# Kernel tuning notes

Measured on AMD Instinct MI355X. Metric: run time of the kernel, lower is better.

## Reference

```python
import jax, jax.numpy as jnp
import numpy as np

N = 50000


def gcn_conv(x, edge_index, W, b):
    # x: [N, F_in], edge_index: [2, E] (row=source j, col=target i)
    n = x.shape[0]
    loops = jnp.arange(n, dtype=edge_index.dtype)
    row = jnp.concatenate([edge_index[0], loops])
    col = jnp.concatenate([edge_index[1], loops])
    # linear transform first (PyG GCNConv)
    xw = x @ W  # [N, F_out]
    # symmetric normalization deg^{-1/2}[row] * deg^{-1/2}[col]
    deg = jax.ops.segment_sum(jnp.ones_like(col, dtype=xw.dtype), col, num_segments=n)
    dis = jnp.where(deg > 0, jax.lax.rsqrt(jnp.maximum(deg, 1e-12)), 0.0)
    norm = dis[row] * dis[col]  # [E+N]
    # gather-scale-scatter: sum_j norm_ij * (W x_j)
    msgs = xw[row] * norm[:, None]
    out = jax.ops.segment_sum(msgs, col, num_segments=n)
    return out + b


def setup_inputs() -> dict:
    key = jax.random.key(0)
    k1, k2, k3, k4, k5 = jax.random.split(key, 5)
    in_dim, hidden_dim, out_dim = 128, 128, 64
    x = jax.random.normal(k1, (N, in_dim), dtype=jnp.float32)
    edge_index = jax.random.randint(k2, (2, 800000), 0, N, dtype=jnp.int64)
    s1 = 1.0 / np.sqrt(in_dim)
    s2 = 1.0 / np.sqrt(hidden_dim)
    W1 = jax.random.uniform(k3, (in_dim, hidden_dim), jnp.float32, -s1, s1)
    b1 = jnp.zeros((hidden_dim,), jnp.float32)
    W2 = jax.random.uniform(k4, (hidden_dim, out_dim), jnp.float32, -s2, s2)
    b2 = jnp.zeros((out_dim,), jnp.float32)
    return {"x": x, "edge_index": edge_index, "W1": W1, "b1": b1, "W2": W2, "b2": b2}


def reference(x, edge_index, W1, b1, W2, b2):
    h = gcn_conv(x, edge_index, W1, b1)
    h = jax.nn.relu(h)
    # dropout(p=0.5, training=False) -> identity (inference reference)
    out = gcn_conv(h, edge_index, W2, b2)
    return out
```

## Files before the change

### kernel.cpp

```cpp
#include <hip/hip_runtime.h>
#include <hip/hip_fp16.h>


typedef _Float16 half8 __attribute__((ext_vector_type(8)));
typedef float floatx4 __attribute__((ext_vector_type(4)));

__global__ void k_count(const int* __restrict__ col, int* __restrict__ deg,
                        int* __restrict__ rank, int E) {
    int e = blockIdx.x * blockDim.x + threadIdx.x;
    if (e < E) rank[e] = atomicAdd(&deg[col[e]], 1);
}

__global__ __launch_bounds__(1024) void k_scan_local(const int* __restrict__ deg,
                                                     int* __restrict__ rowptr,
                                                     int* __restrict__ bsum,
                                                     float* __restrict__ dis, int n) {
    __shared__ int wsum[16];
    int b = blockIdx.x, tid = threadIdx.x;
    int lane = tid & 63, w = tid >> 6;
    int i = b * 1024 + tid;
    int v = (i < n) ? deg[i] : 0;
    if (i < n) dis[i] = rsqrtf((float)v + 1.0f);
    int sc = v;
#pragma unroll
    for (int off = 1; off < 64; off <<= 1) {
        int t = __shfl_up(sc, off);
        if (lane >= off) sc += t;
    }
    if (lane == 63) wsum[w] = sc;
    __syncthreads();
    if (w == 0) {
        int s = (lane < 16) ? wsum[lane] : 0;
#pragma unroll
        for (int off = 1; off < 16; off <<= 1) {
            int t = __shfl_up(s, off);
            if (lane >= off) s += t;
        }
        if (lane < 16) wsum[lane] = s;
    }
    __syncthreads();
    int incl = sc + ((w > 0) ? wsum[w - 1] : 0);
    if (i < n) rowptr[i + 1] = incl;
    if (tid == 1023) bsum[b] = incl;
    if (b == 0 && tid == 0) rowptr[0] = 0;
}

template <int N, typename AT>
__device__ __forceinline__ void gemm_tile(const AT* __restrict__ X,
                                          const float* __restrict__ W,
                                          const float* __restrict__ scale,
                                          __half* __restrict__ Y, int M,
                                          int m0, __half2* wt, int tid) {
    for (int i = tid; i < N * 64; i += 256) {
        int nn = i & (N - 1);
        int k2 = i / N;
        float w0 = W[(size_t)(2 * k2) * N + nn];
        float w1 = W[(size_t)(2 * k2 + 1) * N + nn];
        wt[nn * 64 + ((k2 >> 2) ^ (nn & 15)) * 4 + (k2 & 3)] = __floats2half2_rn(w0, w1);
    }
    __syncthreads();
    int wid = tid >> 6, lane = tid & 63;
    int col = lane & 15, quad = lane >> 4;
    int m_a = m0 + wid * 16 + col;
    bool a_ok = m_a < M;
    constexpr int NT = N / 16;
    floatx4 acc[NT] = {};
#pragma unroll
    for (int ks = 0; ks < 4; ++ks) {
        int k = ks * 32 + quad * 8;
        half8 af;
        if constexpr (sizeof(AT) == 4) {
            floatx4 a0 = {0.f, 0.f, 0.f, 0.f}, a1 = {0.f, 0.f, 0.f, 0.f};
            if (a_ok) {
                a0 = *(const floatx4*)&X[(size_t)m_a * 128 + k];
                a1 = *(const floatx4*)&X[(size_t)m_a * 128 + k + 4];
            }
            af = half8{(_Float16)a0[0], (_Float16)a0[1], (_Float16)a0[2], (_Float16)a0[3],
                       (_Float16)a1[0], (_Float16)a1[1], (_Float16)a1[2], (_Float16)a1[3]};
        } else {
            half8 t = {};
            if (a_ok) t = *(const half8*)(const void*)&X[(size_t)m_a * 128 + k];
            af = t;
        }
        int kblk = ks * 4 + quad;
#pragma unroll
        for (int nt = 0; nt < NT; ++nt) {
            int nn = nt * 16 + col;
            half8 bf = *(const half8*)(const void*)&wt[nn * 64 + (kblk ^ (nn & 15)) * 4];
            acc[nt] = __builtin_amdgcn_mfma_f32_16x16x32_f16(af, bf, acc[nt], 0, 0, 0);
        }
    }
    int mbase = m0 + wid * 16 + quad * 4;
    float s[4];
#pragma unroll
    for (int r = 0; r < 4; ++r) s[r] = (mbase + r < M) ? scale[mbase + r] : 0.f;
#pragma unroll
    for (int nt = 0; nt < NT; ++nt) {
#pragma unroll
        for (int r = 0; r < 4; ++r) {
            if (mbase + r < M)
                Y[(size_t)(mbase + r) * N + nt * 16 + col] = __float2half(acc[nt][r] * s[r]);
        }
    }
}

__global__ __launch_bounds__(256) void k_fix_gemm1(int* __restrict__ rowptr,
                                                   const int* __restrict__ bsum, int n,
                                                   const float* __restrict__ X,
                                                   const float* __restrict__ W,
                                                   const float* __restrict__ scale,
                                                   __half* __restrict__ Y, int M, int FB) {
    __shared__ __align__(16) __half2 wt[128 * 64];
    int b = blockIdx.x, tid = threadIdx.x;
    if (b < FB) {
        int* red = (int*)wt;
        int partial = 0;
        for (int j = tid; j < b; j += 256) partial += bsum[j];
        red[tid] = partial;
        __syncthreads();
        for (int off = 128; off > 0; off >>= 1) {
            if (tid < off) red[tid] += red[tid + off];
            __syncthreads();
        }
        int offv = red[0];
        if (offv == 0) return;
#pragma unroll
        for (int r = 0; r < 4; ++r) {
            int i = b * 1024 + r * 256 + tid;
            if (i < n) rowptr[i + 1] += offv;
        }
        return;
    }
    gemm_tile<128, float>(X, W, scale, Y, M, (b - FB) * 64, wt, tid);
}

__global__ __launch_bounds__(256) void k_gemm2(const __half* __restrict__ X,
                                               const float* __restrict__ W,
                                               const float* __restrict__ scale,
                                               __half* __restrict__ Y, int M) {
    __shared__ __align__(16) __half2 wt[64 * 64];
    gemm_tile<64, __half>(X, W, scale, Y, M, blockIdx.x * 64, wt, threadIdx.x);
}

__global__ void k_fill(const int* __restrict__ row, const int* __restrict__ col,
                       const int* __restrict__ rowptr, const int* __restrict__ rank,
                       int* __restrict__ csr, int E) {
    int e = blockIdx.x * blockDim.x + threadIdx.x;
    if (e < E) csr[rowptr[col[e]] + rank[e]] = row[e];
}

__global__ __launch_bounds__(256) void k_agg128(const __half* __restrict__ xw,
                                                const float* __restrict__ dis,
                                                const int* __restrict__ rowptr,
                                                const int* __restrict__ csr,
                                                const float* __restrict__ bias,
                                                __half* __restrict__ out, int n) {
    int tid = threadIdx.x;
    int lane = tid & 63;
    int q = lane >> 4, li = lane & 15;
    int qbase = lane & 48;
    int node = blockIdx.x * 16 + ((tid >> 6) << 2) + q;
    bool ok = node < n;
    float di = 0.f;
    int beg = 0, end = 0;
    if (ok) {
        di = dis[node];
        beg = rowptr[node];
        end = rowptr[node + 1];
    }
    int dg = end - beg;
    int m1 = max(dg, __shfl(dg, lane ^ 16));
    int mx = max(m1, __shfl(m1, lane ^ 32));
    const half8* rows = (const half8*)xw;
    float acc[8] = {};
    if (ok) {
        half8 sf = rows[(size_t)node * 16 + li];
#pragma unroll
        for (int f = 0; f < 8; ++f) acc[f] = (float)sf[f];
    }
    for (int i = 0; i < mx; i += 8) {
        int e = beg + i + (li & 7);
        int myidx = (e < end) ? csr[e] : 0;
        half8 v[8];
#pragma unroll
        for (int j = 0; j < 8; ++j) {
            int s = __shfl(myidx, qbase + j);
            v[j] = rows[(size_t)s * 16 + li];
        }
#pragma unroll
        for (int j = 0; j < 8; ++j) {
            if (beg + i + j < end) {
#pragma unroll
                for (int f = 0; f < 8; ++f) acc[f] += (float)v[j][f];
            }
        }
    }
    if (ok) {
        floatx4 b0 = *(const floatx4*)&bias[li * 8];
        floatx4 b1 = *(const floatx4*)&bias[li * 8 + 4];
        half8 o;
#pragma unroll
        for (int f = 0; f < 4; ++f) o[f] = (_Float16)fmaxf(acc[f] * di + b0[f], 0.f);
#pragma unroll
        for (int f = 0; f < 4; ++f) o[4 + f] = (_Float16)fmaxf(acc[4 + f] * di + b1[f], 0.f);
        ((half8*)out)[(size_t)node * 16 + li] = o;
    }
}

__global__ __launch_bounds__(256) void k_agg64(const __half* __restrict__ xw,
                                               const float* __restrict__ dis,
                                               const int* __restrict__ rowptr,
                                               const int* __restrict__ csr,
                                               const float* __restrict__ bias,
                                               float* __restrict__ out, int n) {
    int tid = threadIdx.x;
    int lane = tid & 63;
    int o8 = lane >> 3, li = lane & 7;
    int obase = lane & 56;
    int node = blockIdx.x * 32 + ((tid >> 6) << 3) + o8;
    bool ok = node < n;
    float di = 0.f;
    int beg = 0, end = 0;
    if (ok) {
        di = dis[node];
        beg = rowptr[node];
        end = rowptr[node + 1];
    }
    int dg = end - beg;
    int m1 = max(dg, __shfl(dg, lane ^ 8));
    int m2 = max(m1, __shfl(m1, lane ^ 16));
    int mx = max(m2, __shfl(m2, lane ^ 32));
    const half8* rows = (const half8*)xw;
    float acc[8] = {};
    if (ok) {
        half8 sf = rows[(size_t)node * 8 + li];
#pragma unroll
        for (int f = 0; f < 8; ++f) acc[f] = (float)sf[f];
    }
    for (int i = 0; i < mx; i += 8) {
        int e = beg + i + li;
        int myidx = (e < end) ? csr[e] : 0;
        half8 v[8];
#pragma unroll
        for (int j = 0; j < 8; ++j) {
            int s = __shfl(myidx, obase + j);
            v[j] = rows[(size_t)s * 8 + li];
        }
#pragma unroll
        for (int j = 0; j < 8; ++j) {
            if (beg + i + j < end) {
#pragma unroll
                for (int f = 0; f < 8; ++f) acc[f] += (float)v[j][f];
            }
        }
    }
    if (ok) {
        floatx4 b0 = *(const floatx4*)&bias[li * 8];
        floatx4 b1 = *(const floatx4*)&bias[li * 8 + 4];
        floatx4 o0, o1;
#pragma unroll
        for (int f = 0; f < 4; ++f) o0[f] = acc[f] * di + b0[f];
#pragma unroll
        for (int f = 0; f < 4; ++f) o1[f] = acc[4 + f] * di + b1[f];
        *(floatx4*)&out[(size_t)node * 64 + li * 8] = o0;
        *(floatx4*)&out[(size_t)node * 64 + li * 8 + 4] = o1;
    }
}

extern "C" void kernel_launch(void* const* d_in, const int* in_sizes, int n_in,
                              void* d_out, int out_size, void* d_ws, size_t ws_size,
                              hipStream_t stream) {
    const float* x  = (const float*)d_in[0];
    const int*   ei = (const int*)d_in[1];
    const float* W1 = (const float*)d_in[2];
    const float* b1 = (const float*)d_in[3];
    const float* W2 = (const float*)d_in[4];
    const float* b2 = (const float*)d_in[5];
    float* out = (float*)d_out;

    const int n = in_sizes[0] / 128;
    const int E = in_sizes[1] / 2;
    const int* row = ei;
    const int* col = ei + E;
    const int NB = (n + 1023) / 1024;
    const int CB = (E + 255) / 256;
    const int GB = (n + 63) / 64;

    char* ws = (char*)d_ws;
    size_t off = 0;
    auto alloc = [&](size_t bytes) -> void* {
        void* p = ws + off;
        off += (bytes + 255) & ~(size_t)255;
        return p;
    };
    int*    deg    = (int*)alloc((size_t)n * 4);
    int*    rowptr = (int*)alloc((size_t)(n + 1) * 4);
    int*    bsum   = (int*)alloc((size_t)NB * 4);
    int*    rank   = (int*)alloc((size_t)E * 4);
    int*    csr    = (int*)alloc((size_t)E * 4);
    float*  dis    = (float*)alloc((size_t)n * 4);
    __half* xw1    = (__half*)alloc((size_t)n * 128 * 2);
    __half* h      = (__half*)alloc((size_t)n * 128 * 2);
    __half* xw2    = (__half*)alloc((size_t)n * 64 * 2);
    (void)ws_size;

    hipMemsetAsync(deg, 0, (size_t)n * 4, stream);
    k_count<<<CB, 256, 0, stream>>>(col, deg, rank, E);
    k_scan_local<<<NB, 1024, 0, stream>>>(deg, rowptr, bsum, dis, n);
    k_fix_gemm1<<<NB + GB, 256, 0, stream>>>(rowptr, bsum, n, x, W1, dis, xw1, n, NB);
    k_fill<<<CB, 256, 0, stream>>>(row, col, rowptr, rank, csr, E);

    k_agg128<<<(n + 15) / 16, 256, 0, stream>>>(xw1, dis, rowptr, csr, b1, h, n);
    k_gemm2<<<GB, 256, 0, stream>>>(h, W2, dis, xw2, n);
    k_agg64<<<(n + 31) / 32, 256, 0, stream>>>(xw2, dis, rowptr, csr, b2, out, n);
}
```

Before: 203.2 us.

## Slice feature matrices into 16-column planes for cache-friendly gather aggregation

The GEMM outputs are now stored in a sliced layout, with 16 feature columns per plane laid out contiguously across all nodes. Each aggregation block handles one slice for a chunk of nodes, so the gathered working set per slice is smaller and more likely to stay in cache. Within a node group, lanes split the edges and then combine partial sums with xor shuffles. Index loads and output stores use nontemporal hints. The trade-off is that the CSR index loads and degree work are repeated for every slice, and the block-to-slice mapping adds some complexity.

```diff
diff --git a/kernel.cpp b/kernel.cpp
--- a/kernel.cpp
+++ b/kernel.cpp
@@ -45,7 +45,7 @@
     if (b == 0 && tid == 0) rowptr[0] = 0;
 }
 
-template <int N, typename AT>
+template <int N, typename AT, bool SA>
 __device__ __forceinline__ void gemm_tile(const AT* __restrict__ X,
                                           const float* __restrict__ W,
                                           const float* __restrict__ scale,
@@ -77,6 +77,12 @@
             }
             af = half8{(_Float16)a0[0], (_Float16)a0[1], (_Float16)a0[2], (_Float16)a0[3],
                        (_Float16)a1[0], (_Float16)a1[1], (_Float16)a1[2], (_Float16)a1[3]};
+        } else if constexpr (SA) {
+            int slice = ks * 2 + (quad >> 1);
+            half8 t = {};
+            if (a_ok)
+                t = *(const half8*)(const void*)&X[((size_t)slice * M + m_a) * 16 + (quad & 1) * 8];
+            af = t;
         } else {
             half8 t = {};
             if (a_ok) t = *(const half8*)(const void*)&X[(size_t)m_a * 128 + k];
@@ -99,7 +105,7 @@
 #pragma unroll
         for (int r = 0; r < 4; ++r) {
             if (mbase + r < M)
-                Y[(size_t)(mbase + r) * N + nt * 16 + col] = __float2half(acc[nt][r] * s[r]);
+                Y[((size_t)nt * M + (mbase + r)) * 16 + col] = __float2half(acc[nt][r] * s[r]);
         }
     }
 }
@@ -131,7 +137,7 @@
         }
         return;
     }
-    gemm_tile<128, float>(X, W, scale, Y, M, (b - FB) * 64, wt, tid);
+    gemm_tile<128, float, false>(X, W, scale, Y, M, (b - FB) * 64, wt, tid);
 }
 
 __global__ __launch_bounds__(256) void k_gemm2(const __half* __restrict__ X,
@@ -139,7 +145,7 @@
                                                const float* __restrict__ scale,
                                                __half* __restrict__ Y, int M) {
     __shared__ __align__(16) __half2 wt[64 * 64];
-    gemm_tile<64, __half>(X, W, scale, Y, M, blockIdx.x * 64, wt, threadIdx.x);
+    gemm_tile<64, __half, true>(X, W, scale, Y, M, blockIdx.x * 64, wt, threadIdx.x);
 }
 
 __global__ void k_fill(const int* __restrict__ row, const int* __restrict__ col,
@@ -149,17 +155,19 @@
     if (e < E) csr[rowptr[col[e]] + rank[e]] = row[e];
 }
 
-__global__ __launch_bounds__(256) void k_agg128(const __half* __restrict__ xw,
-                                                const float* __restrict__ dis,
-                                                const int* __restrict__ rowptr,
-                                                const int* __restrict__ csr,
-                                                const float* __restrict__ bias,
-                                                __half* __restrict__ out, int n) {
-    int tid = threadIdx.x;
-    int lane = tid & 63;
+__global__ __launch_bounds__(256) void k_agg1s(const __half* __restrict__ xw,
+                                               const float* __restrict__ dis,
+                                               const int* __restrict__ rowptr,
+                                               const int* __restrict__ csr,
+                                               const float* __restrict__ bias,
+                                               __half* __restrict__ h,
+                                               int n) {
+    int b = blockIdx.x;
+    int s = b & 7, chunk = b >> 3;
+    int tid = threadIdx.x, lane = tid & 63;
     int q = lane >> 4, li = lane & 15;
     int qbase = lane & 48;
-    int node = blockIdx.x * 16 + ((tid >> 6) << 2) + q;
+    int node = chunk * 16 + ((tid >> 6) << 2) + q;
     bool ok = node < n;
     float di = 0.f;
     int beg = 0, end = 0;
@@ -171,53 +179,51 @@
     int dg = end - beg;
     int m1 = max(dg, __shfl(dg, lane ^ 16));
     int mx = max(m1, __shfl(m1, lane ^ 32));
-    const half8* rows = (const half8*)xw;
+    const half8* rows = (const half8*)(xw + (size_t)s * n * 16);
+    int pr = li >> 1, hi = li & 1;
     float acc[8] = {};
-    if (ok) {
-        half8 sf = rows[(size_t)node * 16 + li];
-#pragma unroll
-        for (int f = 0; f < 8; ++f) acc[f] = (float)sf[f];
-    }
     for (int i = 0; i < mx; i += 8) {
         int e = beg + i + (li & 7);
-        int myidx = (e < end) ? csr[e] : 0;
-        half8 v[8];
-#pragma unroll
-        for (int j = 0; j < 8; ++j) {
-            int s = __shfl(myidx, qbase + j);
-            v[j] = rows[(size_t)s * 16 + li];
-        }
-#pragma unroll
-        for (int j = 0; j < 8; ++j) {
-            if (beg + i + j < end) {
-#pragma unroll
-                for (int f = 0; f < 8; ++f) acc[f] += (float)v[j][f];
-            }
-        }
-    }
-    if (ok) {
-        floatx4 b0 = *(const floatx4*)&bias[li * 8];
-        floatx4 b1 = *(const floatx4*)&bias[li * 8 + 4];
+        int myidx = (li < 8 && e < end) ? __builtin_nontemporal_load(&csr[e]) : 0;
+        int sj = __shfl(myidx, qbase + pr);
+        half8 v = rows[(size_t)sj * 2 + hi];
+        float m = ((beg + i + pr) < end) ? 1.f : 0.f;
+#pragma unroll
+        for (int f = 0; f < 8; ++f) acc[f] += m * (float)v[f];
+    }
+#pragma unroll
+    for (int off = 2; off <= 8; off <<= 1) {
+#pragma unroll
+        for (int f = 0; f < 8; ++f) acc[f] += __shfl_xor(acc[f], off);
+    }
+    if (ok && li < 2) {
+        half8 sf = rows[(size_t)node * 2 + li];
+        floatx4 b0 = *(const floatx4*)&bias[s * 16 + li * 8];
+        floatx4 b1 = *(const floatx4*)&bias[s * 16 + li * 8 + 4];
         half8 o;
 #pragma unroll
-        for (int f = 0; f < 4; ++f) o[f] = (_Float16)fmaxf(acc[f] * di + b0[f], 0.f);
-#pragma unroll
-        for (int f = 0; f < 4; ++f) o[4 + f] = (_Float16)fmaxf(acc[4 + f] * di + b1[f], 0.f);
-        ((half8*)out)[(size_t)node * 16 + li] = o;
-    }
-}
-
-__global__ __launch_bounds__(256) void k_agg64(const __half* __restrict__ xw,
+        for (int f = 0; f < 4; ++f)
+            o[f] = (_Float16)fmaxf((acc[f] + (float)sf[f]) * di + b0[f], 0.f);
+#pragma unroll
+        for (int f = 0; f < 4; ++f)
+            o[4 + f] = (_Float16)fmaxf((acc[4 + f] + (float)sf[4 + f]) * di + b1[f], 0.f);
+        __builtin_nontemporal_store(
+            o, (half8*)(h + ((size_t)s * n + node) * 16 + li * 8));
+    }
+}
+
+__global__ __launch_bounds__(256) void k_agg2s(const __half* __restrict__ xw,
                                                const float* __restrict__ dis,
                                                const int* __restrict__ rowptr,
                                                const int* __restrict__ csr,
                                                const float* __restrict__ bias,
                                                float* __restrict__ out, int n) {
-    int tid = threadIdx.x;
-    int lane = tid & 63;
-    int o8 = lane >> 3, li = lane & 7;
-    int obase = lane & 56;
-    int node = blockIdx.x * 32 + ((tid >> 6) << 3) + o8;
+    int b = blockIdx.x;
+    int s = (b & 7) >> 1, chunk = ((b >> 3) << 1) | (b & 1);
+    int tid = threadIdx.x, lane = tid & 63;
+    int q = lane >> 4, li = lane & 15;
+    int qbase = lane & 48;
+    int node = chunk * 16 + ((tid >> 6) << 2) + q;
     bool ok = node < n;
     float di = 0.f;
     int beg = 0, end = 0;
@@ -227,43 +233,37 @@
         end = rowptr[node + 1];
     }
     int dg = end - beg;
-    int m1 = max(dg, __shfl(dg, lane ^ 8));
-    int m2 = max(m1, __shfl(m1, lane ^ 16));
-    int mx = max(m2, __shfl(m2, lane ^ 32));
-    const half8* rows = (const half8*)xw;
+    int m1 = max(dg, __shfl(dg, lane ^ 16));
+    int mx = max(m1, __shfl(m1, lane ^ 32));
+    const half8* rows = (const half8*)(xw + (size_t)s * n * 16);
+    int pr = li >> 1, hi = li & 1;
     float acc[8] = {};
-    if (ok) {
-        half8 sf = rows[(size_t)node * 8 + li];
-#pragma unroll
-        for (int f = 0; f < 8; ++f) acc[f] = (float)sf[f];
-    }
     for (int i = 0; i < mx; i += 8) {
-        int e = beg + i + li;
-        int myidx = (e < end) ? csr[e] : 0;
-        half8 v[8];
-#pragma unroll
-        for (int j = 0; j < 8; ++j) {
-            int s = __shfl(myidx, obase + j);
-            v[j] = rows[(size_t)s * 8 + li];
-        }
-#pragma unroll
-        for (int j = 0; j < 8; ++j) {
-            if (beg + i + j < end) {
-#pragma unroll
-                for (int f = 0; f < 8; ++f) acc[f] += (float)v[j][f];
-            }
-        }
-    }
-    if (ok) {
-        floatx4 b0 = *(const floatx4*)&bias[li * 8];
-        floatx4 b1 = *(const floatx4*)&bias[li * 8 + 4];
+        int e = beg + i + (li & 7);
+        int myidx = (li < 8 && e < end) ? __builtin_nontemporal_load(&csr[e]) : 0;
+        int sj = __shfl(myidx, qbase + pr);
+        half8 v = rows[(size_t)sj * 2 + hi];
+        float m = ((beg + i + pr) < end) ? 1.f : 0.f;
+#pragma unroll
+        for (int f = 0; f < 8; ++f) acc[f] += m * (float)v[f];
+    }
+#pragma unroll
+    for (int off = 2; off <= 8; off <<= 1) {
+#pragma unroll
+        for (int f = 0; f < 8; ++f) acc[f] += __shfl_xor(acc[f], off);
+    }
+    if (ok && li < 2) {
+        half8 sf = rows[(size_t)node * 2 + li];
+        floatx4 b0 = *(const floatx4*)&bias[s * 16 + li * 8];
+        floatx4 b1 = *(const floatx4*)&bias[s * 16 + li * 8 + 4];
         floatx4 o0, o1;
 #pragma unroll
-        for (int f = 0; f < 4; ++f) o0[f] = acc[f] * di + b0[f];
-#pragma unroll
-        for (int f = 0; f < 4; ++f) o1[f] = acc[4 + f] * di + b1[f];
-        *(floatx4*)&out[(size_t)node * 64 + li * 8] = o0;
-        *(floatx4*)&out[(size_t)node * 64 + li * 8 + 4] = o1;
+        for (int f = 0; f < 4; ++f) o0[f] = (acc[f] + (float)sf[f]) * di + b0[f];
+#pragma unroll
+        for (int f = 0; f < 4; ++f) o1[f] = (acc[4 + f] + (float)sf[4 + f]) * di + b1[f];
+        float* dst = out + (size_t)node * 64 + s * 16 + li * 8;
+        __builtin_nontemporal_store(o0, (floatx4*)dst);
+        __builtin_nontemporal_store(o1, (floatx4*)(dst + 4));
     }
 }
 
@@ -285,6 +285,7 @@
     const int NB = (n + 1023) / 1024;
     const int CB = (E + 255) / 256;
     const int GB = (n + 63) / 64;
+    const int NCH = (n + 15) / 16;
 
     char* ws = (char*)d_ws;
     size_t off = 0;
@@ -310,7 +311,7 @@
     k_fix_gemm1<<<NB + GB, 256, 0, stream>>>(rowptr, bsum, n, x, W1, dis, xw1, n, NB);
     k_fill<<<CB, 256, 0, stream>>>(row, col, rowptr, rank, csr, E);
 
-    k_agg128<<<(n + 15) / 16, 256, 0, stream>>>(xw1, dis, rowptr, csr, b1, h, n);
+    k_agg1s<<<NCH * 8, 256, 0, stream>>>(xw1, dis, rowptr, csr, b1, h, n);
     k_gemm2<<<GB, 256, 0, stream>>>(h, W2, dis, xw2, n);
-    k_agg64<<<(n + 31) / 32, 256, 0, stream>>>(xw2, dis, rowptr, csr, b2, out, n);
-}
+    k_agg2s<<<((NCH + 1) / 2) * 8, 256, 0, stream>>>(xw2, dis, rowptr, csr, b2, out, n);
+}
```

New measurement: 264.4 us. 1.3x slower.

## Fuse CSR fill into fixup/GEMM1 kernel using raw prefix plus block offsets

Applied to the files above, without the earlier changes.

Removes the separate CSR fill kernel and appends fill blocks to the fixup/GEMM1 launch. Each fill block recomputes the block-sum prefix in shared memory and combines it with a copy of the unfixed local scan (praw), so it no longer depends on the fixup blocks finishing. This saves one launch and lets the scatter overlap with the GEMM, at the cost of an extra rowptr copy and a redundant small scan in every fill block. The scan only covers 64 block sums, which limits n to about 64K nodes.

```diff
diff --git a/kernel.cpp b/kernel.cpp
--- a/kernel.cpp
+++ b/kernel.cpp
@@ -13,6 +13,7 @@
 
 __global__ __launch_bounds__(1024) void k_scan_local(const int* __restrict__ deg,
                                                      int* __restrict__ rowptr,
+                                                     int* __restrict__ praw,
                                                      int* __restrict__ bsum,
                                                      float* __restrict__ dis, int n) {
     __shared__ int wsum[16];
@@ -40,9 +41,15 @@
     }
     __syncthreads();
     int incl = sc + ((w > 0) ? wsum[w - 1] : 0);
-    if (i < n) rowptr[i + 1] = incl;
+    if (i < n) {
+        rowptr[i + 1] = incl;
+        praw[i + 1] = incl;
+    }
     if (tid == 1023) bsum[b] = incl;
-    if (b == 0 && tid == 0) rowptr[0] = 0;
+    if (b == 0 && tid == 0) {
+        rowptr[0] = 0;
+        praw[0] = 0;
+    }
 }
 
 template <int N, typename AT>
@@ -104,12 +111,18 @@
     }
 }
 
-__global__ __launch_bounds__(256) void k_fix_gemm1(int* __restrict__ rowptr,
-                                                   const int* __restrict__ bsum, int n,
-                                                   const float* __restrict__ X,
-                                                   const float* __restrict__ W,
-                                                   const float* __restrict__ scale,
-                                                   __half* __restrict__ Y, int M, int FB) {
+__global__ __launch_bounds__(256) void k_fused(int* __restrict__ rowptr,
+                                               const int* __restrict__ bsum, int n,
+                                               const float* __restrict__ X,
+                                               const float* __restrict__ W,
+                                               const float* __restrict__ scale,
+                                               __half* __restrict__ Y, int M,
+                                               int FB, int GB,
+                                               const int* __restrict__ praw,
+                                               const int* __restrict__ row,
+                                               const int* __restrict__ col,
+                                               const int* __restrict__ rank,
+                                               int* __restrict__ csr, int E) {
     __shared__ __align__(16) __half2 wt[128 * 64];
     int b = blockIdx.x, tid = threadIdx.x;
     if (b < FB) {
@@ -131,6 +144,31 @@
         }
         return;
     }
+    if (b >= FB + GB) {
+        int* q = (int*)wt;
+        int nb = (n + 1023) >> 10;
+        if (tid < 64) {
+            int v = (tid >= 1 && tid <= nb) ? bsum[tid - 1] : 0;
+#pragma unroll
+            for (int off = 1; off < 64; off <<= 1) {
+                int t = __shfl_up(v, off);
+                if ((tid & 63) >= off) v += t;
+            }
+            q[tid] = v;
+        }
+        __syncthreads();
+        int base = (b - FB - GB) * 1024;
+#pragma unroll
+        for (int r = 0; r < 4; ++r) {
+            int e = base + r * 256 + tid;
+            if (e < E) {
+                int c = col[e];
+                int qi = (c == 0) ? 0 : ((c - 1) >> 10);
+                csr[praw[c] + q[qi] + rank[e]] = row[e];
+            }
+        }
+        return;
+    }
     gemm_tile<128, float>(X, W, scale, Y, M, (b - FB) * 64, wt, tid);
 }
 
@@ -140,13 +178,6 @@
                                                __half* __restrict__ Y, int M) {
     __shared__ __align__(16) __half2 wt[64 * 64];
     gemm_tile<64, __half>(X, W, scale, Y, M, blockIdx.x * 64, wt, threadIdx.x);
-}
-
-__global__ void k_fill(const int* __restrict__ row, const int* __restrict__ col,
-                       const int* __restrict__ rowptr, const int* __restrict__ rank,
-                       int* __restrict__ csr, int E) {
-    int e = blockIdx.x * blockDim.x + threadIdx.x;
-    if (e < E) csr[rowptr[col[e]] + rank[e]] = row[e];
 }
 
 __global__ __launch_bounds__(256) void k_agg128(const __half* __restrict__ xw,
@@ -285,6 +316,7 @@
     const int NB = (n + 1023) / 1024;
     const int CB = (E + 255) / 256;
     const int GB = (n + 63) / 64;
+    const int FILLB = (E + 1023) / 1024;
 
     char* ws = (char*)d_ws;
     size_t off = 0;
@@ -295,6 +327,7 @@
     };
     int*    deg    = (int*)alloc((size_t)n * 4);
     int*    rowptr = (int*)alloc((size_t)(n + 1) * 4);
+    int*    praw   = (int*)alloc((size_t)(n + 1) * 4);
     int*    bsum   = (int*)alloc((size_t)NB * 4);
     int*    rank   = (int*)alloc((size_t)E * 4);
     int*    csr    = (int*)alloc((size_t)E * 4);
@@ -306,10 +339,10 @@
 
     hipMemsetAsync(deg, 0, (size_t)n * 4, stream);
     k_count<<<CB, 256, 0, stream>>>(col, deg, rank, E);
-    k_scan_local<<<NB, 1024, 0, stream>>>(deg, rowptr, bsum, dis, n);
-    k_fix_gemm1<<<NB + GB, 256, 0, stream>>>(rowptr, bsum, n, x, W1, dis, xw1, n, NB);
-    k_fill<<<CB, 256, 0, stream>>>(row, col, rowptr, rank, csr, E);
-
+    k_scan_local<<<NB, 1024, 0, stream>>>(deg, rowptr, praw, bsum, dis, n);
+    k_fused<<<NB + GB + FILLB, 256, 0, stream>>>(rowptr, bsum, n, x, W1, dis, xw1,
+                                                 n, NB, GB, praw, row, col, rank,
+                                                 csr, E);
     k_agg128<<<(n + 15) / 16, 256, 0, stream>>>(xw1, dis, rowptr, csr, b1, h, n);
     k_gemm2<<<GB, 256, 0, stream>>>(h, W2, dis, xw2, n);
     k_agg64<<<(n + 31) / 32, 256, 0, stream>>>(xw2, dis, rowptr, csr, b2, out, n);
```

Result: no change. 201.8 us (-0.7%).
